# Kernel optimization log

Hardware: AMD Instinct MI355X
Metric: run time of the kernel (lower is better)

Reference implementation:

```python
import jax, jax.numpy as jnp
import numpy as np

DEPTH = 4
CH = 3
SIG_CHANNELS = 3 + 9 + 27 + 81  # signatory.signature_channels(3, 4) = 120


def _tp(a, b):
    # flattened tensor (outer) product: (N, p) x (N, q) -> (N, p*q), row-major (signatory ordering)
    return (a[:, :, None] * b[:, None, :]).reshape(a.shape[0], -1)


def _signature(path):
    """Depth-4 path signature of path: (N, T, 3) -> (N, 120).

    Segment signature of a linear piece with increment dx is exp(dx):
    levels dx^{otimes k} / k!. Segments are combined with Chen's identity
    via a lax.scan over the time axis.
    """
    dx = path[:, 1:, :] - path[:, :-1, :]  # (N, T-1, 3)
    N, Tm1, _ = dx.shape
    dt = path.dtype
    # per-segment signature levels (flattened)
    s1 = dx                                                                # (N,T-1,3)
    s2 = (s1[..., :, None] * dx[..., None, :]).reshape(N, Tm1, 9) / 2.0   # dx^2/2!
    s3 = (s2[..., :, None] * dx[..., None, :]).reshape(N, Tm1, 27) / 3.0  # dx^3/3!
    s4 = (s3[..., :, None] * dx[..., None, :]).reshape(N, Tm1, 81) / 4.0  # dx^4/4!
    segs = (jnp.moveaxis(s1, 1, 0), jnp.moveaxis(s2, 1, 0),
            jnp.moveaxis(s3, 1, 0), jnp.moveaxis(s4, 1, 0))  # time-leading for scan

    init = (jnp.zeros((N, 3), dt), jnp.zeros((N, 9), dt),
            jnp.zeros((N, 27), dt), jnp.zeros((N, 81), dt))

    def chen_step(carry, seg):
        c1, c2, c3, c4 = carry
        g1, g2, g3, g4 = seg
        n1 = c1 + g1
        n2 = c2 + _tp(c1, g1) + g2
        n3 = c3 + _tp(c2, g1) + _tp(c1, g2) + g3
        n4 = c4 + _tp(c3, g1) + _tp(c2, g2) + _tp(c1, g3) + g4
        return (n1, n2, n3, n4), None

    (c1, c2, c3, c4), _ = jax.lax.scan(chen_step, init, segs)
    return jnp.concatenate([c1, c2, c3, c4], axis=1)  # (N, 120)


def setup_inputs() -> dict:
    key = jax.random.key(0)
    k1, k2, k3, k4, k5 = jax.random.split(key, 5)
    B, T, V, M = 64, 300, 17, 2
    inp = jax.random.normal(k1, (B, CH, T, V, M), dtype=jnp.float32)
    fan1 = 34 * SIG_CHANNELS  # 4080
    W1 = jax.random.uniform(k2, (512, fan1), jnp.float32, -1.0, 1.0) / np.sqrt(fan1)
    b1 = jax.random.uniform(k3, (512,), jnp.float32, -1.0, 1.0) / np.sqrt(fan1)
    W2 = jax.random.uniform(k4, (155, 512), jnp.float32, -1.0, 1.0) / np.sqrt(512)
    b2 = jax.random.uniform(k5, (155,), jnp.float32, -1.0, 1.0) / np.sqrt(512)
    return {"inp": inp, "W1": W1, "b1": b1, "W2": W2, "b2": b2}


def reference(inp, W1, b1, W2, b2):
    B, _, T, V, M = inp.shape
    # order matches the torch loop: for v in range(17): for m in range(2)
    paths = jnp.transpose(inp, (0, 3, 4, 2, 1)).reshape(B * V * M, T, CH)  # (B*34, T, 3)
    sig = _signature(paths).reshape(B, V * M * SIG_CHANNELS)  # (B, 4080)
    h = sig @ W1.T + b1  # dropout is identity in eval mode
    return h @ W2.T + b2  # (B, 155)
```

## Files before the change

kernel.cpp:

```cpp
#include <hip/hip_runtime.h>
#include <hip/hip_bf16.h>

#define B_SZ 64
#define T_PTS 300
#define N_SEG 299
#define VM 34
#define NPATH (B_SZ*VM)
#define SIGC 120
#define FAN1 4080
#define H1 512
#define NOUT 155
#define CHUNK 5
#define KSPL 48
#define KW 85
#define JPW 8

__device__ __forceinline__ void sig_append(float a1[3], float a2[9], float a3[27], float a4[81],
                                           float d0, float d1, float d2) {
  const float d[3] = {d0, d1, d2};

  float Z[3], Y[9], X[27];
#pragma unroll
  for (int i = 0; i < 3; i++) Z[i] = fmaf(d[i], 1.0f / 24.0f, (1.0f / 6.0f) * a1[i]);
#pragma unroll
  for (int e = 0; e < 9; e++) Y[e] = fmaf(d[e % 3], Z[e / 3], 0.5f * a2[e]);
#pragma unroll
  for (int e = 0; e < 27; e++) X[e] = fmaf(d[e % 3], Y[e / 3], a3[e]);
#pragma unroll
  for (int e = 0; e < 81; e++) a4[e] = fmaf(d[e % 3], X[e / 3], a4[e]);

  float Z3[3], Y3[9];
#pragma unroll
  for (int i = 0; i < 3; i++) Z3[i] = fmaf(d[i], 1.0f / 6.0f, 0.5f * a1[i]);
#pragma unroll
  for (int e = 0; e < 9; e++) Y3[e] = fmaf(d[e % 3], Z3[e / 3], a2[e]);
#pragma unroll
  for (int e = 0; e < 27; e++) a3[e] = fmaf(d[e % 3], Y3[e / 3], a3[e]);

  float Z2[3];
#pragma unroll
  for (int i = 0; i < 3; i++) Z2[i] = fmaf(d[i], 0.5f, a1[i]);
#pragma unroll
  for (int e = 0; e < 9; e++) a2[e] = fmaf(d[e % 3], Z2[e / 3], a2[e]);

#pragma unroll
  for (int i = 0; i < 3; i++) a1[i] += d[i];
}

template <int OFF>
__device__ __forceinline__ float lane_down(float x) {
  if constexpr (OFF < 16) {
    return __int_as_float(__builtin_amdgcn_update_dpp(
        0, __float_as_int(x), 0x100 + OFF , 0xF, 0xF, true));
  } else {
    return __shfl_xor(x, OFF);
  }
}

template <int OFF>
__device__ __forceinline__ void chen_round(float a1[3], float a2[9], float a3[27], float a4[81]) {
  float B1[3], B2[9], B3[27];
#pragma unroll
  for (int i = 0; i < 3; i++) B1[i] = lane_down<OFF>(a1[i]);
#pragma unroll
  for (int i = 0; i < 9; i++) B2[i] = lane_down<OFF>(a2[i]);
#pragma unroll
  for (int i = 0; i < 27; i++) B3[i] = lane_down<OFF>(a3[i]);

#pragma unroll
  for (int e = 0; e < 81; e++) {
    const float b4 = lane_down<OFF>(a4[e]);
    float v = a4[e] + b4;
    v = fmaf(a3[e / 3], B1[e % 3], v);
    v = fmaf(a2[e / 9], B2[e % 9], v);
    v = fmaf(a1[e / 27], B3[e % 27], v);
    a4[e] = v;
  }
#pragma unroll
  for (int e = 0; e < 27; e++) {
    float v = a3[e] + B3[e];
    v = fmaf(a2[e / 3], B1[e % 3], v);
    v = fmaf(a1[e / 9], B2[e % 9], v);
    a3[e] = v;
  }
#pragma unroll
  for (int e = 0; e < 9; e++) a2[e] = fmaf(a1[e / 3], B1[e % 3], a2[e] + B2[e]);
#pragma unroll
  for (int i = 0; i < 3; i++) a1[i] += B1[i];
}

__global__ __launch_bounds__(64)
__attribute__((amdgpu_waves_per_eu(1)))
void sig_kernel(const float* __restrict__ inp, float* __restrict__ St,
                float* __restrict__ ht) {
  const int lane = threadIdx.x & 63;
  const int p = blockIdx.x;
  if (p < H1) ht[(size_t)p * 64 + lane] = 0.0f;

  const int b = p / VM;
  const int vm = p - b * VM;
  const int t0 = lane * CHUNK;

  const float* base = inp + (size_t)b * 3 * T_PTS * VM + vm;

  int tv[CHUNK + 1];
#pragma unroll
  for (int s = 0; s <= CHUNK; s++) {
    const int t = t0 + s;
    tv[s] = t < N_SEG ? t : N_SEG;
  }

  float a1[3], a2[9], a3[27], a4[81];
#pragma unroll
  for (int i = 0; i < 3; i++) a1[i] = 0.f;
#pragma unroll
  for (int i = 0; i < 9; i++) a2[i] = 0.f;
#pragma unroll
  for (int i = 0; i < 27; i++) a3[i] = 0.f;
#pragma unroll
  for (int i = 0; i < 81; i++) a4[i] = 0.f;

  float x0 = base[0 * T_PTS * VM + tv[0] * VM];
  float x1 = base[1 * T_PTS * VM + tv[0] * VM];
  float x2 = base[2 * T_PTS * VM + tv[0] * VM];
#pragma unroll
  for (int s = 0; s < CHUNK; s++) {
    const float y0 = base[0 * T_PTS * VM + tv[s + 1] * VM];
    const float y1 = base[1 * T_PTS * VM + tv[s + 1] * VM];
    const float y2 = base[2 * T_PTS * VM + tv[s + 1] * VM];
    const bool valid = (t0 + s) < N_SEG;
    const float d0 = valid ? (y0 - x0) : 0.0f;
    const float d1 = valid ? (y1 - x1) : 0.0f;
    const float d2 = valid ? (y2 - x2) : 0.0f;
    sig_append(a1, a2, a3, a4, d0, d1, d2);
    x0 = y0; x1 = y1; x2 = y2;
  }

  chen_round<1>(a1, a2, a3, a4);
  chen_round<2>(a1, a2, a3, a4);
  chen_round<4>(a1, a2, a3, a4);
  chen_round<8>(a1, a2, a3, a4);
  chen_round<16>(a1, a2, a3, a4);
  chen_round<32>(a1, a2, a3, a4);

  if (lane == 0) {
    float* dst = St + (size_t)(vm * SIGC) * 64 + b;
#pragma unroll
    for (int i = 0; i < 3; i++) dst[(size_t)i * 64] = a1[i];
#pragma unroll
    for (int i = 0; i < 9; i++) dst[(size_t)(3 + i) * 64] = a2[i];
#pragma unroll
    for (int i = 0; i < 27; i++) dst[(size_t)(12 + i) * 64] = a3[i];
#pragma unroll
    for (int i = 0; i < 81; i++) dst[(size_t)(39 + i) * 64] = a4[i];
  }
}

__global__ __launch_bounds__(256) void gemm1_kernel(const float* __restrict__ St,
                                                    const float* __restrict__ W1,
                                                    float* __restrict__ ht) {
  const int lane = threadIdx.x & 63;
  int wave_id = (blockIdx.x * 256 + threadIdx.x) >> 6;
  wave_id = __builtin_amdgcn_readfirstlane(wave_id);
  const int ks = wave_id >> 6;
  const int jg = wave_id & 63;
  const int k0 = ks * KW;

  const float* stp = St + (size_t)k0 * 64 + lane;
  const float* w[JPW];
#pragma unroll
  for (int r = 0; r < JPW; r++) w[r] = W1 + (size_t)(jg * JPW + r) * FAN1 + k0;

  float sv[KW];
#pragma unroll
  for (int i = 0; i < KW; i++) sv[i] = stp[(size_t)i * 64];

  float acc[JPW];
#pragma unroll
  for (int r = 0; r < JPW; r++) acc[r] = 0.f;

#pragma unroll
  for (int i = 0; i < KW; i++) {
#pragma unroll
    for (int r = 0; r < JPW; r++) acc[r] = fmaf(sv[i], w[r][i], acc[r]);
  }

  float* hp = ht + (size_t)(jg * JPW) * 64 + lane;
#pragma unroll
  for (int r = 0; r < JPW; r++) atomicAdd(hp + r * 64, acc[r]);
}

__global__ __launch_bounds__(256) void gemm2_kernel(const float* __restrict__ ht,
                                                    const float* __restrict__ W2,
                                                    const float* __restrict__ b1,
                                                    const float* __restrict__ b2,
                                                    float* __restrict__ out) {
  const int j = blockIdx.x;
  const int lane = threadIdx.x & 63;
  int w = threadIdx.x >> 6;
  w = __builtin_amdgcn_readfirstlane(w);
  __shared__ float red[4][64];

  const float* htp = ht + (size_t)(w * 128) * 64 + lane;
  const float* w2r = W2 + (size_t)j * H1 + w * 128;
  const float* b1r = b1 + w * 128;
  float acc = 0.f, accb = 0.f;
#pragma unroll 8
  for (int k = 0; k < 128; k++) {
    const float wv = w2r[k];
    acc = fmaf(wv, htp[(size_t)k * 64], acc);
    accb = fmaf(wv, b1r[k], accb);
  }

  red[w][lane] = acc + accb;
  __syncthreads();
  if (threadIdx.x < 64) {
    const float tot = red[0][lane] + red[1][lane] + red[2][lane] + red[3][lane];
    out[(size_t)lane * NOUT + j] = tot + b2[j];
  }
}

extern "C" void kernel_launch(void* const* d_in, const int* in_sizes, int n_in,
                              void* d_out, int out_size, void* d_ws, size_t ws_size,
                              hipStream_t stream) {
  const float* inp = (const float*)d_in[0];
  const float* W1  = (const float*)d_in[1];
  const float* b1  = (const float*)d_in[2];
  const float* W2  = (const float*)d_in[3];
  const float* b2  = (const float*)d_in[4];
  float* out = (float*)d_out;

  float* St = (float*)d_ws;
  float* ht = St + (size_t)FAN1 * 64;

  sig_kernel<<<NPATH, 64, 0, stream>>>(inp, St, ht);
  gemm1_kernel<<<KSPL * 64 / 4, 256, 0, stream>>>(St, W1, ht);
  gemm2_kernel<<<NOUT, 256, 0, stream>>>(ht, W2, b1, b2, out);
}
```

Baseline: 114.2 us.

## Finish cross-lane Chen reduction in LDS with element-parallel combines

The last two Chen-identity combine rounds (lane offsets 16 and 32) no longer use a full 120-element cross-lane shuffle with redundant per-lane compute. The four partial signatures held by lanes 0/16/32/48 are written to shared memory and combined in a two-level tree. Each lane computes two output elements using precomputed index and mask tables. This removes about 240 ds_bpermute shuffles and several hundred redundant FMAs per lane, at the cost of two block barriers and scattered LDS reads. The final signature is now written to global memory by all lanes instead of by lane 0 alone.

```diff
diff --git a/kernel.cpp b/kernel.cpp
--- a/kernel.cpp
+++ b/kernel.cpp
@@ -49,12 +49,8 @@
 
 template <int OFF>
 __device__ __forceinline__ float lane_down(float x) {
-  if constexpr (OFF < 16) {
-    return __int_as_float(__builtin_amdgcn_update_dpp(
-        0, __float_as_int(x), 0x100 + OFF , 0xF, 0xF, true));
-  } else {
-    return __shfl_xor(x, OFF);
-  }
+  return __int_as_float(__builtin_amdgcn_update_dpp(
+      0, __float_as_int(x), 0x100 + OFF , 0xF, 0xF, true));
 }
 
 template <int OFF>
@@ -93,6 +89,7 @@
 __attribute__((amdgpu_waves_per_eu(1)))
 void sig_kernel(const float* __restrict__ inp, float* __restrict__ St,
                 float* __restrict__ ht) {
+  __shared__ float smem[6 * 128];
   const int lane = threadIdx.x & 63;
   const int p = blockIdx.x;
   if (p < H1) ht[(size_t)p * 64 + lane] = 0.0f;
@@ -140,20 +137,74 @@
   chen_round<2>(a1, a2, a3, a4);
   chen_round<4>(a1, a2, a3, a4);
   chen_round<8>(a1, a2, a3, a4);
-  chen_round<16>(a1, a2, a3, a4);
-  chen_round<32>(a1, a2, a3, a4);
-
-  if (lane == 0) {
+
+  if ((lane & 15) == 0) {
+    float* s = smem + (lane >> 4) * 128;
+#pragma unroll
+    for (int i = 0; i < 3; i++) s[i] = a1[i];
+#pragma unroll
+    for (int i = 0; i < 9; i++) s[3 + i] = a2[i];
+#pragma unroll
+    for (int i = 0; i < 27; i++) s[12 + i] = a3[i];
+#pragma unroll
+    for (int i = 0; i < 81; i++) s[39 + i] = a4[i];
+  }
+  __syncthreads();
+
+  int o1a[2], o1b[2], o2a[2], o2b[2], o3a[2], o3b[2];
+  float m2[2], m3[2], m4[2];
+#pragma unroll
+  for (int q = 0; q < 2; q++) {
+    const int g = 2 * lane + q;
+    o1a[q] = o1b[q] = o2a[q] = o2b[q] = o3a[q] = o3b[q] = 0;
+    m2[q] = m3[q] = m4[q] = 0.f;
+    if (g >= 39 && g < 120) {
+      const int e = g - 39;
+      o1a[q] = 12 + e / 3;  o1b[q] = e % 3;       m2[q] = 1.f;
+      o2a[q] = 3 + e / 9;   o2b[q] = 3 + e % 9;   m3[q] = 1.f;
+      o3a[q] = e / 27;      o3b[q] = 12 + e % 27; m4[q] = 1.f;
+    } else if (g >= 12 && g < 39) {
+      const int e = g - 12;
+      o1a[q] = 3 + e / 3;   o1b[q] = e % 3;       m2[q] = 1.f;
+      o2a[q] = e / 9;       o2b[q] = 3 + e % 9;   m3[q] = 1.f;
+    } else if (g >= 3 && g < 12) {
+      const int e = g - 3;
+      o1a[q] = e / 3;       o1b[q] = e % 3;       m2[q] = 1.f;
+    }
+  }
+  const int g0 = 2 * lane, g1 = 2 * lane + 1;
+
+#define CHEN_ELEM(Aoff, Boff, g, q, dstvar)                                       \
+  do {                                                                            \
+    float c_ = smem[(Aoff) + (g)] + smem[(Boff) + (g)];                           \
+    c_ = fmaf(m2[q] * smem[(Aoff) + o1a[q]], smem[(Boff) + o1b[q]], c_);          \
+    c_ = fmaf(m3[q] * smem[(Aoff) + o2a[q]], smem[(Boff) + o2b[q]], c_);          \
+    c_ = fmaf(m4[q] * smem[(Aoff) + o3a[q]], smem[(Boff) + o3b[q]], c_);          \
+    dstvar = c_;                                                                  \
+  } while (0)
+
+  {
+    float v0, v1, w0, w1;
+    CHEN_ELEM(0 * 128, 1 * 128, g0, 0, v0);
+    CHEN_ELEM(0 * 128, 1 * 128, g1, 1, v1);
+    CHEN_ELEM(2 * 128, 3 * 128, g0, 0, w0);
+    CHEN_ELEM(2 * 128, 3 * 128, g1, 1, w1);
+    smem[4 * 128 + g0] = v0;
+    smem[4 * 128 + g1] = v1;
+    smem[5 * 128 + g0] = w0;
+    smem[5 * 128 + g1] = w1;
+  }
+  __syncthreads();
+
+  {
+    float v0, v1;
+    CHEN_ELEM(4 * 128, 5 * 128, g0, 0, v0);
+    CHEN_ELEM(4 * 128, 5 * 128, g1, 1, v1);
     float* dst = St + (size_t)(vm * SIGC) * 64 + b;
-#pragma unroll
-    for (int i = 0; i < 3; i++) dst[(size_t)i * 64] = a1[i];
-#pragma unroll
-    for (int i = 0; i < 9; i++) dst[(size_t)(3 + i) * 64] = a2[i];
-#pragma unroll
-    for (int i = 0; i < 27; i++) dst[(size_t)(12 + i) * 64] = a3[i];
-#pragma unroll
-    for (int i = 0; i < 81; i++) dst[(size_t)(39 + i) * 64] = a4[i];
-  }
+    if (g0 < SIGC) dst[(size_t)g0 * 64] = v0;
+    if (g1 < SIGC) dst[(size_t)g1 * 64] = v1;
+  }
+#undef CHEN_ELEM
 }
 
 __global__ __launch_bounds__(256) void gemm1_kernel(const float* __restrict__ St,
```

New measurement: 115.5 us. Within noise of the previous version (+1.1%).

## Split each path across two waves and finish Chen combine in shared memory

Applied to the files above, without the earlier changes.

The signature kernel now uses 128 threads per path with 3 segments each instead of 64 threads with 5. The in-register butterfly Chen reduction stops at 16-lane groups, so only DPP shuffles are used. The remaining 8 partial signatures are combined by a three-level tree in LDS, with each thread computing one signature element. The aim is to shorten the per-thread serial append chain and raise occupancy via waves_per_eu(3). The cost is extra LDS traffic, barriers and divergent per-element index math.

```diff
diff --git a/kernel.cpp b/kernel.cpp
--- a/kernel.cpp
+++ b/kernel.cpp
@@ -10,7 +10,7 @@
 #define FAN1 4080
 #define H1 512
 #define NOUT 155
-#define CHUNK 5
+#define CHUNK 3
 #define KSPL 48
 #define KW 85
 #define JPW 8
@@ -49,12 +49,8 @@
 
 template <int OFF>
 __device__ __forceinline__ float lane_down(float x) {
-  if constexpr (OFF < 16) {
-    return __int_as_float(__builtin_amdgcn_update_dpp(
-        0, __float_as_int(x), 0x100 + OFF , 0xF, 0xF, true));
-  } else {
-    return __shfl_xor(x, OFF);
-  }
+  return __int_as_float(__builtin_amdgcn_update_dpp(
+      0, __float_as_int(x), 0x100 + OFF , 0xF, 0xF, true));
 }
 
 template <int OFF>
@@ -89,27 +85,48 @@
   for (int i = 0; i < 3; i++) a1[i] += B1[i];
 }
 
-__global__ __launch_bounds__(64)
-__attribute__((amdgpu_waves_per_eu(1)))
+__device__ __forceinline__ float chen_elem(const float* __restrict__ A,
+                                           const float* __restrict__ Bv, int g) {
+  int a1o = 0, b1o = 0, a2o = 0, b2o = 0, a3o = 0, b3o = 0;
+  float m1 = 0.f, m2 = 0.f, m3 = 0.f;
+  if (g >= 39) {
+    const int e = g - 39;
+    a1o = 12 + e / 3;  b1o = e % 3;       m1 = 1.f;
+    a2o = 3 + e / 9;   b2o = 3 + e % 9;   m2 = 1.f;
+    a3o = e / 27;      b3o = 12 + e % 27; m3 = 1.f;
+  } else if (g >= 12) {
+    const int e = g - 12;
+    a1o = 3 + e / 3;   b1o = e % 3;       m1 = 1.f;
+    a2o = e / 9;       b2o = 3 + e % 9;   m2 = 1.f;
+  } else if (g >= 3) {
+    const int e = g - 3;
+    a1o = e / 3;       b1o = e % 3;       m1 = 1.f;
+  }
+  float c = A[g] + Bv[g];
+  c = fmaf(m1 * A[a1o], Bv[b1o], c);
+  c = fmaf(m2 * A[a2o], Bv[b2o], c);
+  c = fmaf(m3 * A[a3o], Bv[b3o], c);
+  return c;
+}
+
+__global__ __launch_bounds__(128)
+__attribute__((amdgpu_waves_per_eu(3)))
 void sig_kernel(const float* __restrict__ inp, float* __restrict__ St,
                 float* __restrict__ ht) {
-  const int lane = threadIdx.x & 63;
+  __shared__ float smem[14 * 128];
+  const int tid = threadIdx.x;
+  const int lane = tid & 63;
+  const int wv = tid >> 6;
   const int p = blockIdx.x;
-  if (p < H1) ht[(size_t)p * 64 + lane] = 0.0f;
+  if (p < 256) ht[(size_t)p * 128 + tid] = 0.0f;
 
   const int b = p / VM;
   const int vm = p - b * VM;
-  const int t0 = lane * CHUNK;
+  const int gl = wv * 64 + lane;
+  const int t0 = gl * CHUNK;
 
   const float* base = inp + (size_t)b * 3 * T_PTS * VM + vm;
 
-  int tv[CHUNK + 1];
-#pragma unroll
-  for (int s = 0; s <= CHUNK; s++) {
-    const int t = t0 + s;
-    tv[s] = t < N_SEG ? t : N_SEG;
-  }
-
   float a1[3], a2[9], a3[27], a4[81];
 #pragma unroll
   for (int i = 0; i < 3; i++) a1[i] = 0.f;
@@ -120,14 +137,16 @@
 #pragma unroll
   for (int i = 0; i < 81; i++) a4[i] = 0.f;
 
-  float x0 = base[0 * T_PTS * VM + tv[0] * VM];
-  float x1 = base[1 * T_PTS * VM + tv[0] * VM];
-  float x2 = base[2 * T_PTS * VM + tv[0] * VM];
+  const int tp0 = t0 < N_SEG ? t0 : N_SEG;
+  float x0 = base[0 * T_PTS * VM + tp0 * VM];
+  float x1 = base[1 * T_PTS * VM + tp0 * VM];
+  float x2 = base[2 * T_PTS * VM + tp0 * VM];
 #pragma unroll
   for (int s = 0; s < CHUNK; s++) {
-    const float y0 = base[0 * T_PTS * VM + tv[s + 1] * VM];
-    const float y1 = base[1 * T_PTS * VM + tv[s + 1] * VM];
-    const float y2 = base[2 * T_PTS * VM + tv[s + 1] * VM];
+    const int tn = (t0 + s + 1) < N_SEG ? (t0 + s + 1) : N_SEG;
+    const float y0 = base[0 * T_PTS * VM + tn * VM];
+    const float y1 = base[1 * T_PTS * VM + tn * VM];
+    const float y2 = base[2 * T_PTS * VM + tn * VM];
     const bool valid = (t0 + s) < N_SEG;
     const float d0 = valid ? (y0 - x0) : 0.0f;
     const float d1 = valid ? (y1 - x1) : 0.0f;
@@ -140,19 +159,51 @@
   chen_round<2>(a1, a2, a3, a4);
   chen_round<4>(a1, a2, a3, a4);
   chen_round<8>(a1, a2, a3, a4);
-  chen_round<16>(a1, a2, a3, a4);
-  chen_round<32>(a1, a2, a3, a4);
-
-  if (lane == 0) {
-    float* dst = St + (size_t)(vm * SIGC) * 64 + b;
-#pragma unroll
-    for (int i = 0; i < 3; i++) dst[(size_t)i * 64] = a1[i];
-#pragma unroll
-    for (int i = 0; i < 9; i++) dst[(size_t)(3 + i) * 64] = a2[i];
-#pragma unroll
-    for (int i = 0; i < 27; i++) dst[(size_t)(12 + i) * 64] = a3[i];
-#pragma unroll
-    for (int i = 0; i < 81; i++) dst[(size_t)(39 + i) * 64] = a4[i];
+
+  if ((lane & 15) == 0) {
+    float* s = smem + (wv * 4 + (lane >> 4)) * 128;
+#pragma unroll
+    for (int i = 0; i < 3; i++) s[i] = a1[i];
+#pragma unroll
+    for (int i = 0; i < 9; i++) s[3 + i] = a2[i];
+#pragma unroll
+    for (int i = 0; i < 27; i++) s[12 + i] = a3[i];
+#pragma unroll
+    for (int i = 0; i < 81; i++) s[39 + i] = a4[i];
+  }
+  __syncthreads();
+
+  {
+    const int pr = tid >> 5;
+    const int i0 = tid & 31;
+    const float* A = smem + (2 * pr) * 128;
+    const float* Bv = smem + (2 * pr + 1) * 128;
+    float* D = smem + (8 + pr) * 128;
+#pragma unroll
+    for (int s = 0; s < 4; s++) {
+      const int g = i0 + 32 * s;
+      if (g < SIGC) D[g] = chen_elem(A, Bv, g);
+    }
+  }
+  __syncthreads();
+
+  {
+    const int pr = tid >> 6;
+    const int i0 = tid & 63;
+    const float* A = smem + (8 + 2 * pr) * 128;
+    const float* Bv = smem + (8 + 2 * pr + 1) * 128;
+    float* D = smem + (12 + pr) * 128;
+#pragma unroll
+    for (int s = 0; s < 2; s++) {
+      const int g = i0 + 64 * s;
+      if (g < SIGC) D[g] = chen_elem(A, Bv, g);
+    }
+  }
+  __syncthreads();
+
+  if (tid < SIGC) {
+    const float v = chen_elem(smem + 12 * 128, smem + 13 * 128, tid);
+    St[(size_t)(vm * SIGC + tid) * 64 + b] = v;
   }
 }
 
@@ -233,7 +284,7 @@
   float* St = (float*)d_ws;
   float* ht = St + (size_t)FAN1 * 64;
 
-  sig_kernel<<<NPATH, 64, 0, stream>>>(inp, St, ht);
+  sig_kernel<<<NPATH, 128, 0, stream>>>(inp, St, ht);
   gemm1_kernel<<<KSPL * 64 / 4, 256, 0, stream>>>(St, W1, ht);
   gemm2_kernel<<<NOUT, 256, 0, stream>>>(ht, W2, b1, b2, out);
 }
```

New measurement: 197.8 us. 1.73x slower.
